# Performance work log

Measured on AMD Instinct MI355X. Metric: run time of the kernel, lower is better.

Reference implementation:

```python
import jax, jax.numpy as jnp
import numpy as np


def setup_inputs() -> dict:
    key = jax.random.key(0)
    ks = jax.random.split(key, 4)
    B, T, D, U = 64, 512, 1024, 1024
    scale = 1.0 / np.sqrt(D)
    return {
        "x": jax.random.normal(ks[0], (B, T, D), dtype=jnp.float32),
        "kernel_z": jax.random.normal(ks[1], (D, U), dtype=jnp.float32) * scale,
        "kernel_r": jax.random.normal(ks[2], (D, U), dtype=jnp.float32) * scale,
        "kernel_h": jax.random.normal(ks[3], (D, U), dtype=jnp.float32) * scale,
        "memory_z": jnp.ones((U,), dtype=jnp.float32),
        "memory_r": jnp.ones((U,), dtype=jnp.float32),
        "bias_z": jnp.zeros((U,), dtype=jnp.float32),
        "bias_r": jnp.zeros((U,), dtype=jnp.float32),
        "bias_h": jnp.zeros((U,), dtype=jnp.float32),
    }


def _bru_scan(x, kernel_z, kernel_r, kernel_h, memory_z, memory_r,
              bias_z, bias_r, bias_h):
    B, T, D = x.shape
    U = kernel_z.shape[1]
    # Precompute the three input projections for all timesteps at once
    # (same math as per-step K.dot; hoisted out of the recurrence).
    xz = jnp.einsum('btd,du->btu', x, kernel_z) + bias_z  # [B,T,U]
    xr = jnp.einsum('btd,du->btu', x, kernel_r) + bias_r
    xh = jnp.einsum('btd,du->btu', x, kernel_h) + bias_h

    def step(h, xs):
        xz_t, xr_t, xh_t = xs
        r = jnp.tanh(xr_t + h * memory_r) + 1.0
        z = jax.nn.sigmoid(xz_t + h * memory_z)
        hh = jnp.tanh(xh_t + r * h)
        out = (1.0 - z) * hh + z * h
        return out, out

    h0 = jnp.zeros((B, U), dtype=x.dtype)
    # scan over time axis
    xs = (jnp.swapaxes(xz, 0, 1), jnp.swapaxes(xr, 0, 1), jnp.swapaxes(xh, 0, 1))
    _, outs = jax.lax.scan(step, h0, xs)  # outs: [T,B,U]
    return jnp.swapaxes(outs, 0, 1)  # [B,T,U]


def reference(x, kernel_z, kernel_r, kernel_h, memory_z, memory_r,
              bias_z, bias_r, bias_h):
    return _bru_scan(x, kernel_z, kernel_r, kernel_h, memory_z, memory_r,
                     bias_z, bias_r, bias_h)
```

## Files before the change

kernel.cpp:

```cpp
#include <hip/hip_runtime.h>
#include <cmath>

using f16x8  = __attribute__((ext_vector_type(8))) _Float16;
using f32x16 = __attribute__((ext_vector_type(16))) float;

__device__ __forceinline__ void gld16(void* lds, const void* g) {
    __builtin_amdgcn_global_load_lds(
        (const __attribute__((address_space(1))) unsigned int*)g,
        (__attribute__((address_space(3))) unsigned int*)lds, 16, 0, 0);
}


__global__ __launch_bounds__(256)
void bru_conv_a(const float* __restrict__ x, char* __restrict__ Ablob,
                int T, int D, int Tc, int t0, int Mc)
{
    const int idx = blockIdx.x * 256 + threadIdx.x;
    const int kt = idx / Mc;
    const int m  = idx - kt * Mc;

    const long xrow = (long)(m / Tc) * T + t0 + (m % Tc);
    const float* src = x + xrow * (long)D + kt * 32;

    float v[32];
    #pragma unroll
    for (int i = 0; i < 8; ++i)
        *(float4*)&v[i * 4] = *(const float4*)(src + i * 4);

    #pragma unroll
    for (int q = 0; q < 4; ++q) {
        _Float16 hi[8], lo[8];
        #pragma unroll
        for (int j = 0; j < 8; ++j) {
            float f = v[q * 8 + j];
            hi[j] = (_Float16)f;
            lo[j] = (_Float16)(f - (float)hi[j]);
        }
        char* b0 = Ablob + ((size_t)(kt * 8 + 2 * q) * Mc + m) * 16;
        char* b1 = Ablob + ((size_t)(kt * 8 + 2 * q + 1) * Mc + m) * 16;
        *(f16x8*)b0 = *(f16x8*)hi;
        *(f16x8*)b1 = *(f16x8*)lo;
    }
}

__global__ __launch_bounds__(256)
void bru_conv_w(const float* __restrict__ wz, const float* __restrict__ wr,
                const float* __restrict__ wh, char* __restrict__ Wblob,
                int D, int U)
{
    const int gid  = blockIdx.x * 256 + threadIdx.x;
    const int blob = gid >> 11;
    const int idx  = gid & 2047;
    const int row  = idx >> 3;
    const int s    = idx & 7;

    const int g    = blob >> 6;
    const int rest = blob & 63;
    const int nt   = rest >> 4;
    const int kt2  = rest & 15;

    const float* W = (g == 0) ? wz : (g == 1) ? wr : wh;
    const int q  = s ^ (row & 7);
    const int d0 = kt2 * 64 + q * 8;
    const int u  = nt * 256 + row;

    _Float16 o[8];
    #pragma unroll
    for (int j = 0; j < 8; ++j)
        o[j] = (_Float16)W[(long)(d0 + j) * U + u];

    *(f16x8*)(Wblob + ((size_t)((g * 4 + nt) * 18 + kt2)) * 32768 + row * 128 + s * 16)
        = *(f16x8*)o;
}

__global__ __launch_bounds__(512, 2)
void bru_gemm_mfma(const char* __restrict__ Ablob, const char* __restrict__ Wblob,
                   const float* __restrict__ bz, const float* __restrict__ br,
                   const float* __restrict__ bh,
                   _Float16* __restrict__ proj,
                   int nmt, int U, int Mc)
{
    __shared__ char sm[131072];

    const int ngrid = gridDim.x;
    const int bid   = blockIdx.x;
    int lid = bid;
    if ((ngrid & 7) == 0) lid = (bid & 7) * (ngrid >> 3) + (bid >> 3);
    const int mt  = lid / 12;
    const int rem = lid - mt * 12;
    const int g   = rem >> 2;
    const int nt  = rem & 3;

    const int tid  = threadIdx.x;
    const int lane = tid & 63;
    const int w    = tid >> 6;
    const int wm   = w >> 1, wn = w & 1;
    const int l31  = lane & 31;
    const int lhi  = lane >> 5;
    const int stoff = tid * 16;

    const char* bsrc = Wblob + (size_t)((g * 4 + nt) * 18) * 32768;

    const int arow = mt * 256 + wm * 64 + l31;
    const size_t aMc = (size_t)Mc;
#define AADDR(kt_, q_, i_, lo_) \
    (Ablob + (((size_t)((kt_) * 8 + (q_) * 2 + (lo_))) * aMc + (size_t)(arow + (i_) * 32)) * 16)

    const int brow = wn * 128 + l31;
    const int br7  = brow & 7;
#define BOFF(j_, q_) \
    ((size_t)(brow + (j_) * 32) * 128 + (size_t)(((q_) ^ br7) * 16))

#define STAGE(p_) \
    _Pragma("unroll") for (int i_ = 0; i_ < 4; ++i_) \
        gld16(sm + ((p_) & 3) * 32768 + i_ * 8192 + stoff, \
              bsrc + (size_t)(p_) * 32768 + i_ * 8192 + stoff);

#define LOADA(dst, kt_) \
    _Pragma("unroll") for (int ks_ = 0; ks_ < 2; ++ks_) \
    _Pragma("unroll") for (int i_ = 0; i_ < 2; ++i_) \
    _Pragma("unroll") for (int lo_ = 0; lo_ < 2; ++lo_) \
        dst[ks_][i_][lo_] = *(const f16x8*)AADDR(kt_, ks_ * 2 + lhi, i_, lo_);

#define KSTEP(bufp, par_, ks_, SET) do { \
    __builtin_amdgcn_s_setprio(1); \
    _Pragma("unroll") for (int j_ = 0; j_ < 4; ++j_) { \
        f16x8 wv = *(const f16x8*)((bufp) + BOFF(j_, (par_) * 4 + (ks_) * 2 + lhi)); \
        _Pragma("unroll") for (int i_ = 0; i_ < 2; ++i_) { \
            acc[i_][j_] = __builtin_amdgcn_mfma_f32_32x32x16_f16(SET[ks_][i_][0], wv, acc[i_][j_], 0, 0, 0); \
            acc[i_][j_] = __builtin_amdgcn_mfma_f32_32x32x16_f16(SET[ks_][i_][1], wv, acc[i_][j_], 0, 0, 0); \
        } } \
    __builtin_amdgcn_s_setprio(0); } while (0)

    f32x16 acc[2][4];
    #pragma unroll
    for (int i = 0; i < 2; ++i)
        #pragma unroll
        for (int j = 0; j < 4; ++j) acc[i][j] = (f32x16)0.f;

    f16x8 A0[2][2][2], A1[2][2][2];

    STAGE(0); STAGE(1);
    LOADA(A0, 0);
    __builtin_amdgcn_sched_barrier(0);
    asm volatile("s_waitcnt vmcnt(12)" ::: "memory");
    __builtin_amdgcn_sched_barrier(0);
    __builtin_amdgcn_s_barrier();

    for (int p = 0; p < 16; ++p) {
        const char* buf = sm + (p & 3) * 32768;

        STAGE(p + 2);
        LOADA(A1, 2 * p + 1);

        KSTEP(buf, 0, 0, A0);
        KSTEP(buf, 0, 1, A0);

        LOADA(A0, 2 * p + 2);

        KSTEP(buf, 1, 0, A1);
        KSTEP(buf, 1, 1, A1);

        __builtin_amdgcn_sched_barrier(0);
        asm volatile("s_waitcnt vmcnt(20)" ::: "memory");
        __builtin_amdgcn_sched_barrier(0);
        __builtin_amdgcn_s_barrier();
    }
#undef AADDR
#undef BOFF
#undef STAGE
#undef LOADA
#undef KSTEP

    const float* bias = (g == 0) ? bz : (g == 1) ? br : bh;
    float bcol[4];
    #pragma unroll
    for (int j = 0; j < 4; ++j) bcol[j] = bias[nt * 256 + wn * 128 + j * 32 + l31];

    _Float16* cbase = proj + (size_t)g * Mc * U + (size_t)(nt * 256 + wn * 128) + l31;
    #pragma unroll
    for (int i = 0; i < 2; ++i) {
        #pragma unroll
        for (int j = 0; j < 4; ++j) {
            #pragma unroll
            for (int reg = 0; reg < 16; ++reg) {
                const int row = mt * 256 + wm * 64 + i * 32 + (reg & 3) + 8 * (reg >> 2) + 4 * lhi;
                cbase[(size_t)row * U + j * 32] = (_Float16)(acc[i][j][reg] + bcol[j]);
            }
        }
    }
}

#define PF 8
__global__ __launch_bounds__(256)
void bru_scan(const _Float16* __restrict__ proj,
              const float* __restrict__ mz, const float* __restrict__ mr,
              float* __restrict__ out,
              float* __restrict__ hstate,
              int B, int T, int U, int Tc, int t0, int Mc)
{
    const int idx = blockIdx.x * blockDim.x + threadIdx.x;
    const int b = idx / U;
    const int u = idx - b * U;

    float h = (t0 == 0) ? 0.f : hstate[idx];
    const float vmz = mz[u];
    const float vmr = mr[u];

    const _Float16* pz = proj + (long)b * Tc * U + u;
    const _Float16* pr = pz + (long)Mc * U;
    const _Float16* ph = pr + (long)Mc * U;
    float* po = out + ((long)b * T + t0) * U + u;

    _Float16 fz[PF], fr[PF], fh[PF];
    #pragma unroll
    for (int i = 0; i < PF; ++i) {
        const long o = (long)((i < Tc) ? i : (Tc - 1)) * U;
        fz[i] = pz[o]; fr[i] = pr[o]; fh[i] = ph[o];
    }

    for (int t = 0; t < Tc; t += PF) {
        #pragma unroll
        for (int i = 0; i < PF; ++i) {
            const float xz = (float)fz[i];
            const float xr = (float)fr[i];
            const float xh = (float)fh[i];
            {
                int tn = t + i + PF; if (tn > Tc - 1) tn = Tc - 1;
                const long o = (long)tn * U;
                fz[i] = pz[o]; fr[i] = pr[o]; fh[i] = ph[o];
            }
            const float e2r = __expf(2.f * (xr + h * vmr));
            const float rr  = 2.f - 2.f / (e2r + 1.f);
            const float zz  = 1.f / (1.f + __expf(-(xz + h * vmz)));
            const float e2h = __expf(2.f * (xh + rr * h));
            const float hh  = 1.f - 2.f / (e2h + 1.f);
            h = (1.f - zz) * hh + zz * h;
            if (t + i < Tc) po[(long)(t + i) * U] = h;
        }
    }
    hstate[idx] = h;
}

extern "C" void kernel_launch(void* const* d_in, const int* in_sizes, int n_in,
                              void* d_out, int out_size, void* d_ws, size_t ws_size,
                              hipStream_t stream)
{
    const float* x  = (const float*)d_in[0];
    const float* wz = (const float*)d_in[1];
    const float* wr = (const float*)d_in[2];
    const float* wh = (const float*)d_in[3];
    const float* mz = (const float*)d_in[4];
    const float* mr = (const float*)d_in[5];
    const float* bz = (const float*)d_in[6];
    const float* br = (const float*)d_in[7];
    const float* bh = (const float*)d_in[8];

    const int B = 64, T = 512, D = 1024, U = 1024;

    const size_t h_bytes = (size_t)B * U * sizeof(float);
    const size_t w_bytes = (size_t)12 * 18 * 32768;

    int Tc = T;
    while (Tc > 4) {
        const int Mc_ = B * Tc;
        const size_t a_bytes_ = (size_t)33 * 8 * Mc_ * 16;
        const size_t p_bytes_ = 3ull * Mc_ * U * sizeof(_Float16);
        if (h_bytes + w_bytes + a_bytes_ + p_bytes_ <= ws_size) break;
        Tc >>= 1;
    }
    const int nmt = B * Tc / 256;
    const int Mc  = B * Tc;
    const size_t a_bytes = (size_t)33 * 8 * Mc * 16;

    float*    h_state = (float*)d_ws;
    char*     Wblob   = (char*)d_ws + h_bytes;
    char*     Ablob   = (char*)d_ws + h_bytes + w_bytes;
    _Float16* proj    = (_Float16*)((char*)d_ws + h_bytes + w_bytes + a_bytes);

    bru_conv_w<<<3 * 4 * 16 * 2048 / 256, 256, 0, stream>>>(wz, wr, wh, Wblob, D, U);

    for (int t0 = 0; t0 < T; t0 += Tc) {
        bru_conv_a<<<(Mc * 32) / 256, 256, 0, stream>>>(x, Ablob, T, D, Tc, t0, Mc);

        bru_gemm_mfma<<<3 * nmt * 4, 512, 0, stream>>>(
            Ablob, Wblob, bz, br, bh, proj, nmt, U, Mc);

        bru_scan<<<(B * U) / 256, 256, 0, stream>>>(
            proj, mz, mr, (float*)d_out, h_state, B, T, U, Tc, t0, Mc);
    }
}
```

Baseline: 586.5 us.

## Drop LDS staging in projection GEMM; load weights directly from global per wave

Measured after the change: 829.2 us. 1.41x slower.

```diff
diff --git a/kernel.cpp b/kernel.cpp
--- a/kernel.cpp
+++ b/kernel.cpp
@@ -4,12 +4,8 @@
 using f16x8  = __attribute__((ext_vector_type(8))) _Float16;
 using f32x16 = __attribute__((ext_vector_type(16))) float;
 
-__device__ __forceinline__ void gld16(void* lds, const void* g) {
-    __builtin_amdgcn_global_load_lds(
-        (const __attribute__((address_space(1))) unsigned int*)g,
-        (__attribute__((address_space(3))) unsigned int*)lds, 16, 0, 0);
-}
-
+
+#define WSLICE_STRIDE (132 * 64 * 16)
 
 __global__ __launch_bounds__(256)
 void bru_conv_a(const float* __restrict__ x, char* __restrict__ Ablob,
@@ -48,28 +44,27 @@
                 const float* __restrict__ wh, char* __restrict__ Wblob,
                 int D, int U)
 {
-    const int gid  = blockIdx.x * 256 + threadIdx.x;
-    const int blob = gid >> 11;
-    const int idx  = gid & 2047;
-    const int row  = idx >> 3;
-    const int s    = idx & 7;
-
-    const int g    = blob >> 6;
-    const int rest = blob & 63;
-    const int nt   = rest >> 4;
-    const int kt2  = rest & 15;
+    const int gid   = blockIdx.x * 256 + threadIdx.x;
+    const int slice = gid >> 13;
+    const int idx   = gid & 8191;
+    const int qg    = idx >> 6;
+    const int u     = idx & 63;
+
+    const int g    = slice >> 4;
+    const int rest = slice & 15;
+    const int nt   = rest >> 2;
+    const int sl   = rest & 3;
 
     const float* W = (g == 0) ? wz : (g == 1) ? wr : wh;
-    const int q  = s ^ (row & 7);
-    const int d0 = kt2 * 64 + q * 8;
-    const int u  = nt * 256 + row;
+    const int ucol = nt * 256 + sl * 64 + u;
+    const int d0   = qg * 8;
 
     _Float16 o[8];
     #pragma unroll
     for (int j = 0; j < 8; ++j)
-        o[j] = (_Float16)W[(long)(d0 + j) * U + u];
-
-    *(f16x8*)(Wblob + ((size_t)((g * 4 + nt) * 18 + kt2)) * 32768 + row * 128 + s * 16)
+        o[j] = (_Float16)W[(long)(d0 + j) * U + ucol];
+
+    *(f16x8*)(Wblob + (size_t)slice * WSLICE_STRIDE + ((size_t)qg * 64 + u) * 16)
         = *(f16x8*)o;
 }
 
@@ -80,8 +75,6 @@
                    _Float16* __restrict__ proj,
                    int nmt, int U, int Mc)
 {
-    __shared__ char sm[131072];
-
     const int ngrid = gridDim.x;
     const int bid   = blockIdx.x;
     int lid = bid;
@@ -94,97 +87,79 @@
     const int tid  = threadIdx.x;
     const int lane = tid & 63;
     const int w    = tid >> 6;
-    const int wm   = w >> 1, wn = w & 1;
+    const int wm   = w >> 2, wn = w & 3;
     const int l31  = lane & 31;
     const int lhi  = lane >> 5;
-    const int stoff = tid * 16;
-
-    const char* bsrc = Wblob + (size_t)((g * 4 + nt) * 18) * 32768;
-
-    const int arow = mt * 256 + wm * 64 + l31;
+
+    const char* wsrc = Wblob + (size_t)((g * 4 + nt) * 4 + wn) * WSLICE_STRIDE;
+    const int arow = mt * 256 + wm * 128 + l31;
     const size_t aMc = (size_t)Mc;
-#define AADDR(kt_, q_, i_, lo_) \
-    (Ablob + (((size_t)((kt_) * 8 + (q_) * 2 + (lo_))) * aMc + (size_t)(arow + (i_) * 32)) * 16)
-
-    const int brow = wn * 128 + l31;
-    const int br7  = brow & 7;
-#define BOFF(j_, q_) \
-    ((size_t)(brow + (j_) * 32) * 128 + (size_t)(((q_) ^ br7) * 16))
-
-#define STAGE(p_) \
+
+#define AADDR(K_, i_, lo_) \
+    (Ablob + (((size_t)(((K_) >> 1) * 8 + (((K_) & 1) * 2 + lhi) * 2 + (lo_))) * aMc \
+              + (size_t)(arow + (i_) * 32)) * 16)
+#define WADDR(K_, j_) \
+    (wsrc + ((size_t)((2 * (K_) + lhi) * 64 + (j_) * 32 + l31)) * 16)
+
+#define LOADA(AS, K_) \
     _Pragma("unroll") for (int i_ = 0; i_ < 4; ++i_) \
-        gld16(sm + ((p_) & 3) * 32768 + i_ * 8192 + stoff, \
-              bsrc + (size_t)(p_) * 32768 + i_ * 8192 + stoff);
-
-#define LOADA(dst, kt_) \
-    _Pragma("unroll") for (int ks_ = 0; ks_ < 2; ++ks_) \
-    _Pragma("unroll") for (int i_ = 0; i_ < 2; ++i_) \
     _Pragma("unroll") for (int lo_ = 0; lo_ < 2; ++lo_) \
-        dst[ks_][i_][lo_] = *(const f16x8*)AADDR(kt_, ks_ * 2 + lhi, i_, lo_);
-
-#define KSTEP(bufp, par_, ks_, SET) do { \
+        AS[i_][lo_] = *(const f16x8*)AADDR(K_, i_, lo_);
+
+#define LOADW(WS, K_) \
+    _Pragma("unroll") for (int j_ = 0; j_ < 2; ++j_) \
+        WS[j_] = *(const f16x8*)WADDR(K_, j_);
+
+#define KSTEP(WS, AS) do { \
     __builtin_amdgcn_s_setprio(1); \
-    _Pragma("unroll") for (int j_ = 0; j_ < 4; ++j_) { \
-        f16x8 wv = *(const f16x8*)((bufp) + BOFF(j_, (par_) * 4 + (ks_) * 2 + lhi)); \
-        _Pragma("unroll") for (int i_ = 0; i_ < 2; ++i_) { \
-            acc[i_][j_] = __builtin_amdgcn_mfma_f32_32x32x16_f16(SET[ks_][i_][0], wv, acc[i_][j_], 0, 0, 0); \
-            acc[i_][j_] = __builtin_amdgcn_mfma_f32_32x32x16_f16(SET[ks_][i_][1], wv, acc[i_][j_], 0, 0, 0); \
-        } } \
+    _Pragma("unroll") for (int j_ = 0; j_ < 2; ++j_) \
+    _Pragma("unroll") for (int i_ = 0; i_ < 4; ++i_) \
+        acc[i_][j_] = __builtin_amdgcn_mfma_f32_32x32x16_f16(AS[i_][0], WS[j_], acc[i_][j_], 0, 0, 0); \
+    _Pragma("unroll") for (int j_ = 0; j_ < 2; ++j_) \
+    _Pragma("unroll") for (int i_ = 0; i_ < 4; ++i_) \
+        acc[i_][j_] = __builtin_amdgcn_mfma_f32_32x32x16_f16(AS[i_][1], WS[j_], acc[i_][j_], 0, 0, 0); \
     __builtin_amdgcn_s_setprio(0); } while (0)
 
-    f32x16 acc[2][4];
-    #pragma unroll
-    for (int i = 0; i < 2; ++i)
-        #pragma unroll
-        for (int j = 0; j < 4; ++j) acc[i][j] = (f32x16)0.f;
-
-    f16x8 A0[2][2][2], A1[2][2][2];
-
-    STAGE(0); STAGE(1);
-    LOADA(A0, 0);
-    __builtin_amdgcn_sched_barrier(0);
-    asm volatile("s_waitcnt vmcnt(12)" ::: "memory");
-    __builtin_amdgcn_sched_barrier(0);
-    __builtin_amdgcn_s_barrier();
+    f32x16 acc[4][2];
+    #pragma unroll
+    for (int i = 0; i < 4; ++i)
+        #pragma unroll
+        for (int j = 0; j < 2; ++j) acc[i][j] = (f32x16)0.f;
+
+    f16x8 Ae[4][2], Ao[4][2];
+    f16x8 We[2], Wo[2];
+
+    LOADW(We, 0); LOADW(Wo, 1);
+    LOADA(Ae, 0); LOADA(Ao, 1);
 
     for (int p = 0; p < 16; ++p) {
-        const char* buf = sm + (p & 3) * 32768;
-
-        STAGE(p + 2);
-        LOADA(A1, 2 * p + 1);
-
-        KSTEP(buf, 0, 0, A0);
-        KSTEP(buf, 0, 1, A0);
-
-        LOADA(A0, 2 * p + 2);
-
-        KSTEP(buf, 1, 0, A1);
-        KSTEP(buf, 1, 1, A1);
-
-        __builtin_amdgcn_sched_barrier(0);
-        asm volatile("s_waitcnt vmcnt(20)" ::: "memory");
-        __builtin_amdgcn_sched_barrier(0);
-        __builtin_amdgcn_s_barrier();
+        const int K = 4 * p;
+        KSTEP(We, Ae); LOADW(We, K + 2); LOADA(Ae, K + 2);
+        KSTEP(Wo, Ao); LOADW(Wo, K + 3); LOADA(Ao, K + 3);
+        KSTEP(We, Ae); LOADW(We, K + 4); LOADA(Ae, K + 4);
+        KSTEP(Wo, Ao); LOADW(Wo, K + 5); LOADA(Ao, K + 5);
     }
 #undef AADDR
-#undef BOFF
-#undef STAGE
+#undef WADDR
 #undef LOADA
+#undef LOADW
 #undef KSTEP
 
     const float* bias = (g == 0) ? bz : (g == 1) ? br : bh;
-    float bcol[4];
-    #pragma unroll
-    for (int j = 0; j < 4; ++j) bcol[j] = bias[nt * 256 + wn * 128 + j * 32 + l31];
-
-    _Float16* cbase = proj + (size_t)g * Mc * U + (size_t)(nt * 256 + wn * 128) + l31;
-    #pragma unroll
-    for (int i = 0; i < 2; ++i) {
-        #pragma unroll
-        for (int j = 0; j < 4; ++j) {
+    const int n0 = nt * 256 + wn * 64;
+    float bcol[2];
+    #pragma unroll
+    for (int j = 0; j < 2; ++j) bcol[j] = bias[n0 + j * 32 + l31];
+
+    _Float16* cbase = proj + (size_t)g * Mc * U + (size_t)n0 + l31;
+    #pragma unroll
+    for (int i = 0; i < 4; ++i) {
+        #pragma unroll
+        for (int j = 0; j < 2; ++j) {
             #pragma unroll
             for (int reg = 0; reg < 16; ++reg) {
-                const int row = mt * 256 + wm * 64 + i * 32 + (reg & 3) + 8 * (reg >> 2) + 4 * lhi;
+                const int row = mt * 256 + wm * 128 + i * 32
+                              + (reg & 3) + 8 * (reg >> 2) + 4 * lhi;
                 cbase[(size_t)row * U + j * 32] = (_Float16)(acc[i][j][reg] + bcol[j]);
             }
         }
@@ -259,7 +234,7 @@
     const int B = 64, T = 512, D = 1024, U = 1024;
 
     const size_t h_bytes = (size_t)B * U * sizeof(float);
-    const size_t w_bytes = (size_t)12 * 18 * 32768;
+    const size_t w_bytes = (size_t)48 * WSLICE_STRIDE;
 
     int Tc = T;
     while (Tc > 4) {
@@ -278,7 +253,7 @@
     char*     Ablob   = (char*)d_ws + h_bytes + w_bytes;
     _Float16* proj    = (_Float16*)((char*)d_ws + h_bytes + w_bytes + a_bytes);
 
-    bru_conv_w<<<3 * 4 * 16 * 2048 / 256, 256, 0, stream>>>(wz, wr, wh, Wblob, D, U);
+    bru_conv_w<<<48 * 8192 / 256, 256, 0, stream>>>(wz, wr, wh, Wblob, D, U);
 
     for (int t0 = 0; t0 < T; t0 += Tc) {
         bru_conv_a<<<(Mc * 32) / 256, 256, 0, stream>>>(x, Ablob, T, D, Tc, t0, Mc);
```
